# Performance work log

Measured on AMD Instinct MI355X. Metric: run time of the kernel, lower is better.

## Reference

```python
import jax, jax.numpy as jnp
import numpy as np

NUM_HEADS = 32
ROPE_BASE = 10000.0


def _rotate_half(x):
    h = x.shape[-1] // 2
    return jnp.concatenate([-x[..., h:], x[..., :h]], axis=-1)


def setup_inputs() -> dict:
    key = jax.random.key(0)
    ks = jax.random.split(key, 6)
    B, S, H = 2, 2048, 4096
    hidden_states = jax.random.normal(ks[0], (B, S, H), dtype=jnp.float32)
    # additive causal mask: 0 on/below diagonal, large negative above
    causal = jnp.tril(jnp.ones((S, S), dtype=bool))
    attention_mask = jnp.where(causal, 0.0, -1e9).astype(jnp.float32)
    attention_mask = jnp.broadcast_to(attention_mask[None, None], (B, 1, S, S))
    position_ids = jnp.broadcast_to(jnp.arange(S, dtype=jnp.int64 if jax.config.jax_enable_x64 else jnp.int32)[None, :], (B, S))
    scale = 1.0 / np.sqrt(H)
    Wq = jax.random.normal(ks[1], (H, H), dtype=jnp.float32) * scale
    Wk = jax.random.normal(ks[2], (H, H), dtype=jnp.float32) * scale
    Wv = jax.random.normal(ks[3], (H, H), dtype=jnp.float32) * scale
    Wo = jax.random.normal(ks[4], (H, H), dtype=jnp.float32) * scale
    return {"hidden_states": hidden_states, "attention_mask": attention_mask,
            "position_ids": position_ids, "Wq": Wq, "Wk": Wk, "Wv": Wv, "Wo": Wo}


def reference(hidden_states, attention_mask, position_ids, Wq, Wk, Wv, Wo):
    B, S, H = hidden_states.shape
    nh = NUM_HEADS
    hd = H // nh
    # QKV projections (torch Linear: y = x @ W.T), split heads -> [B, nh, S, hd]
    def proj(W):
        y = jnp.einsum('bsh,oh->bso', hidden_states, W)
        return y.reshape(B, S, nh, hd).transpose(0, 2, 1, 3)
    q, k, v = proj(Wq), proj(Wk), proj(Wv)
    # rotary embeddings gathered at position_ids
    inv_freq = 1.0 / (ROPE_BASE ** (jnp.arange(0, hd, 2, dtype=jnp.float32) / hd))
    freqs = position_ids.astype(jnp.float32)[:, :, None] * inv_freq[None, None, :]  # [B,S,hd/2]
    emb = jnp.concatenate([freqs, freqs], axis=-1)  # [B,S,hd]
    cos = jnp.cos(emb)[:, None, :, :]  # [B,1,S,hd]
    sin = jnp.sin(emb)[:, None, :, :]
    q = q * cos + _rotate_half(q) * sin
    k = k * cos + _rotate_half(k) * sin
    # scaled dot-product attention
    scores = jnp.einsum('bhqd,bhkd->bhqk', q, k) / jnp.sqrt(jnp.float32(hd))
    scores = scores + attention_mask
    scores = jnp.maximum(scores, jnp.finfo(scores.dtype).min)
    attn = jax.nn.softmax(scores, axis=-1)
    out = jnp.einsum('bhqk,bhkd->bhqd', attn, v)  # [B,nh,S,hd]
    out = out.transpose(0, 2, 1, 3).reshape(B, S, H)
    return jnp.einsum('bsh,oh->bso', out, Wo)
```

## Files before the change

kernel.cpp:

```cpp
#include <hip/hip_runtime.h>
#include <cstdint>
#include <cmath>

typedef __bf16 bf16;
typedef __bf16 bf16x8 __attribute__((ext_vector_type(8)));
typedef __bf16 bf16x4 __attribute__((ext_vector_type(4)));
typedef float f32x4 __attribute__((ext_vector_type(4)));

#define B_ 2
#define S_ 2048
#define H_ 4096
#define NH 32
#define HD 128

#define VMCNT(n) asm volatile("s_waitcnt vmcnt(" #n ")" ::: "memory")
#define BAR() __builtin_amdgcn_s_barrier()

__device__ __forceinline__ void gl_lds16(const void* g, void* l) {
  __builtin_amdgcn_global_load_lds(
      (const __attribute__((address_space(1))) unsigned int*)g,
      (__attribute__((address_space(3))) unsigned int*)l, 16, 0, 0);
}

__global__ __launch_bounds__(256) void cast_kernel(const float* __restrict__ in,
                                                   bf16* __restrict__ out, int n4) {
  int i = blockIdx.x * 256 + threadIdx.x;
  if (i < n4) {
    float4 v = ((const float4*)in)[i];
    bf16x4 o = {(bf16)v.x, (bf16)v.y, (bf16)v.z, (bf16)v.w};
    ((bf16x4*)out)[i] = o;
  }
}

template <int TM, int TN>
__device__ __forceinline__ void mfma_quad(f32x4 (&acc)[8][4], bf16x8 (&af)[4][2],
                                          bf16x8 (&bfr)[2][2]) {
  __builtin_amdgcn_s_setprio(1);
#pragma unroll
  for (int i = 0; i < 4; ++i)
#pragma unroll
    for (int j = 0; j < 2; ++j)
#pragma unroll
      for (int kf = 0; kf < 2; ++kf)
        acc[TM * 4 + i][TN * 2 + j] = __builtin_amdgcn_mfma_f32_16x16x32_bf16(
            af[i][kf], bfr[j][kf], acc[TM * 4 + i][TN * 2 + j], 0, 0, 0);
  __builtin_amdgcn_s_setprio(0);
}

template <int EPI>
__global__ __launch_bounds__(512, 2) void gemm256(const bf16* __restrict__ A,
                                                  const bf16* __restrict__ Bw,
                                                  void* __restrict__ Cout) {
  constexpr int K = 4096, N = 4096, KT = K / 64;
  __shared__ __attribute__((aligned(16))) char lds[131072];
  char* Al = lds;
  char* Bl = lds + 65536;
  int tid = threadIdx.x;
  int l = tid & 63, lr = l & 15, lg = l >> 4;
  int w = tid >> 6, wm = w >> 2, wn = w & 3;
  int bid = (int)blockIdx.x;
  int swb = (bid & 7) * 32 + (bid >> 3);
  int r0 = (swb >> 4) * 256, c0 = (swb & 15) * 256;
  const bf16* Ab = A + (size_t)r0 * K;
  const bf16* Bb = Bw + (size_t)c0 * K;

  int lr0 = tid >> 3;
  int cel = (((tid & 7) ^ ((tid >> 3) & 7)) << 3);

  auto stageA = [&](int buf, int mh, int k0) {
    char* dst = Al + buf * 32768 + mh * 16384 + tid * 16;
    int ra = mh * 64 + lr0;
    gl_lds16(Ab + (size_t)ra * K + k0 + cel, dst);
    gl_lds16(Ab + (size_t)(ra + 128) * K + k0 + cel, dst + 8192);
  };
  auto stageB = [&](int buf, int nh, int k0) {
    char* dst = Bl + buf * 32768 + nh * 16384 + tid * 16;
    int n0 = (lr0 >> 5) * 64 + nh * 32 + (lr0 & 31);
    gl_lds16(Bb + (size_t)n0 * K + k0 + cel, dst);
    gl_lds16(Bb + (size_t)(n0 + 128) * K + k0 + cel, dst + 8192);
  };

  bf16x8 af[4][2], bfr[2][2];
  int rsw = (lr & 7) << 4;
  auto ldA = [&](int buf, int mh) {
    char* base = Al + buf * 32768 + mh * 16384 + wm * 8192;
#pragma unroll
    for (int mfl = 0; mfl < 4; ++mfl)
#pragma unroll
      for (int kf = 0; kf < 2; ++kf)
        __builtin_memcpy(&af[mfl][kf],
                         base + (mfl * 16 + lr) * 128 + ((kf * 64 + lg * 16) ^ rsw), 16);
  };
  auto ldB = [&](int buf, int nh) {
    char* base = Bl + buf * 32768 + nh * 16384 + wn * 4096;
#pragma unroll
    for (int nfl = 0; nfl < 2; ++nfl)
#pragma unroll
      for (int kf = 0; kf < 2; ++kf)
        __builtin_memcpy(&bfr[nfl][kf],
                         base + (nfl * 16 + lr) * 128 + ((kf * 64 + lg * 16) ^ rsw), 16);
  };

  f32x4 acc[8][4] = {};

  stageA(0, 0, 0);
  stageB(0, 0, 0);
  stageB(0, 1, 0);
  stageA(0, 1, 0);

  for (int kt = 0; kt < KT - 1; ++kt) {
    int buf = kt & 1, nb = buf ^ 1;
    int k0n = (kt + 1) * 64;
    VMCNT(4); BAR();
    ldA(buf, 0); ldB(buf, 0);
    stageA(nb, 0, k0n);
    mfma_quad<0, 0>(acc, af, bfr);
    BAR();
    VMCNT(4); BAR();
    ldB(buf, 1);
    stageB(nb, 0, k0n);
    mfma_quad<0, 1>(acc, af, bfr);
    BAR();
    VMCNT(4); BAR();
    ldA(buf, 1);
    stageB(nb, 1, k0n);
    mfma_quad<1, 1>(acc, af, bfr);
    BAR();
    BAR();
    ldB(buf, 0);
    stageA(nb, 1, k0n);
    mfma_quad<1, 0>(acc, af, bfr);
    BAR();
  }
  {
    int buf = (KT - 1) & 1;
    VMCNT(4); BAR();
    ldA(buf, 0); ldB(buf, 0);
    mfma_quad<0, 0>(acc, af, bfr);
    BAR();
    VMCNT(2); BAR();
    ldB(buf, 1);
    mfma_quad<0, 1>(acc, af, bfr);
    BAR();
    VMCNT(0); BAR();
    ldA(buf, 1);
    mfma_quad<1, 1>(acc, af, bfr);
    BAR();
    BAR();
    ldB(buf, 0);
    mfma_quad<1, 0>(acc, af, bfr);
  }

#pragma unroll
  for (int mf = 0; mf < 8; ++mf)
#pragma unroll
    for (int nf = 0; nf < 4; ++nf) {
      int orow = r0 + wm * 128 + mf * 16 + lg * 4;
      int ocol = c0 + wn * 64 + nf * 16 + lr;
      if (EPI == 0) {
        bf16* C = (bf16*)Cout;
#pragma unroll
        for (int jr = 0; jr < 4; ++jr)
          C[(size_t)(orow + jr) * N + ocol] = (bf16)acc[mf][nf][jr];
      } else {
        float* C = (float*)Cout;
#pragma unroll
        for (int jr = 0; jr < 4; ++jr)
          C[(size_t)(orow + jr) * N + ocol] = acc[mf][nf][jr];
      }
    }
}

__global__ __launch_bounds__(256) void rope_kernel(bf16* __restrict__ Qx,
                                                   bf16* __restrict__ Kx,
                                                   const int* __restrict__ pos,
                                                   float qscale) {
  int r = blockIdx.x;
  bf16* X = blockIdx.y ? Kx : Qx;
  float scale = blockIdx.y ? 1.0f : qscale;
  float pf = (float)pos[r];
  int i = threadIdx.x & 63;
  int h0 = threadIdx.x >> 6;
  float ang = pf * exp2f(-0.20762050593046868f * (float)i);
  float sn = sinf(ang), cs = cosf(ang);
  bf16* row = X + (size_t)r * H_;
#pragma unroll
  for (int h = h0; h < NH; h += 4) {
    bf16* p = row + h * HD + i;
    float a = (float)p[0], b = (float)p[64];
    p[0] = (bf16)((a * cs - b * sn) * scale);
    p[64] = (bf16)((b * cs + a * sn) * scale);
  }
}

__global__ __launch_bounds__(256) void transpose_v(const bf16* __restrict__ V,
                                                   bf16* __restrict__ Vt) {
  __shared__ __attribute__((aligned(16))) bf16 tile[64][130];
  int bh = blockIdx.y;
  int b = bh >> 5, h = bh & 31;
  int s0 = blockIdx.x * 64;
  int t = threadIdx.x;
  const bf16* src = V + (size_t)(b * S_ + s0) * H_ + h * HD;
  int rr = t >> 4, cc = (t & 15) * 8;
#pragma unroll
  for (int k = 0; k < 4; ++k) {
    bf16x8 v;
    __builtin_memcpy(&v, src + (size_t)(rr + k * 16) * H_ + cc, 16);
#pragma unroll
    for (int u = 0; u < 8; ++u) tile[rr + k * 16][cc + u] = v[u];
  }
  __syncthreads();
  bf16* dst = Vt + (size_t)bh * HD * S_;
  int sl = t & 63, d0 = t >> 6;
  for (int j = 0; j < 32; ++j) {
    int d = d0 + j * 4;
    dst[(size_t)d * S_ + s0 + sl] = tile[sl][d];
  }
}

__global__ __launch_bounds__(512, 4) void attn_kernel(const bf16* __restrict__ Q,
                                                      const bf16* __restrict__ Km,
                                                      const bf16* __restrict__ Vt,
                                                      bf16* __restrict__ Out) {
  __shared__ __attribute__((aligned(16))) bf16 Ks[2][64 * 128];
  __shared__ __attribute__((aligned(16))) bf16 Vs[2][128 * 64];
  __shared__ __attribute__((aligned(16))) bf16 P_lds[8][16 * 64];
  int tid = threadIdx.x;
  int w = tid >> 6, l = tid & 63;
  int lr = l & 15, lg = l >> 4;
  int bh = blockIdx.y, b = bh >> 5, h = bh & 31;
  int qt = 15 - (int)blockIdx.x;
  int q0w = qt * 128 + w * 16;
  const bf16* Qb = Q + (size_t)b * S_ * H_ + h * HD;
  const char* Kg = (const char*)(Km + (size_t)b * S_ * H_ + h * HD);
  const char* Vg = (const char*)(Vt + (size_t)bh * HD * S_);
  bf16* Ob = Out + (size_t)b * S_ * H_ + h * HD;

  bf16x8 qf[4];
#pragma unroll
  for (int dk = 0; dk < 4; ++dk)
    __builtin_memcpy(&qf[dk], Qb + (size_t)(q0w + lr) * H_ + dk * 32 + lg * 8, 16);

  f32x4 o[8] = {};
  float m = -INFINITY, ls = 0.f;
  int nkv_blk = 2 * qt + 2;
  int nkv_w = 2 * qt + (w >> 2) + 1;

  auto stageK = [&](int buf, int kv0) {
#pragma unroll
    for (int p = 0; p < 2; ++p) {
      int row = p * 32 + (tid >> 4);
      int src = ((tid & 15) * 16) ^ ((row & 7) << 4);
      gl_lds16(Kg + (size_t)(kv0 + row) * (H_ * 2) + src,
               (char*)&Ks[buf][0] + p * 8192 + w * 1024);
    }
  };
  auto stageV = [&](int buf, int kv0) {
#pragma unroll
    for (int p = 0; p < 2; ++p) {
      int row = p * 64 + (tid >> 3);
      int src = ((tid & 7) * 16) ^ ((row & 7) << 4);
      gl_lds16(Vg + (size_t)row * (S_ * 2) + (size_t)kv0 * 2 + src,
               (char*)&Vs[buf][0] + p * 8192 + w * 1024);
    }
  };

  stageK(0, 0);
  stageV(0, 0);
  __syncthreads();

  int cur = 0;
  char* Pl = (char*)&P_lds[w][0];
  for (int t = 0; t < nkv_blk; ++t) {
    int kv0 = t * 64;
    if (t + 1 < nkv_blk) {
      stageK(cur ^ 1, kv0 + 64);
      stageV(cur ^ 1, kv0 + 64);
    }
    if (t < nkv_w) {
      const char* Kl = (const char*)&Ks[cur][0];
      const char* Vl = (const char*)&Vs[cur][0];
      f32x4 s4[4] = {};
      __builtin_amdgcn_s_setprio(1);
#pragma unroll
      for (int dk = 0; dk < 4; ++dk)
#pragma unroll
        for (int st = 0; st < 4; ++st) {
          int row = st * 16 + lr;
          int cb = (dk * 64 + lg * 16) ^ ((row & 7) << 4);
          bf16x8 kf;
          __builtin_memcpy(&kf, Kl + row * 256 + cb, 16);
          s4[st] = __builtin_amdgcn_mfma_f32_16x16x32_bf16(kf, qf[dk], s4[st], 0, 0, 0);
        }
      __builtin_amdgcn_s_setprio(0);
      if (t == nkv_w - 1) {
        int qg = q0w + lr;
#pragma unroll
        for (int st = 0; st < 4; ++st)
#pragma unroll
          for (int j = 0; j < 4; ++j)
            if (kv0 + st * 16 + lg * 4 + j > qg) s4[st][j] = -INFINITY;
      }
      float mx = -INFINITY;
#pragma unroll
      for (int st = 0; st < 4; ++st)
#pragma unroll
        for (int j = 0; j < 4; ++j) mx = fmaxf(mx, s4[st][j]);
      mx = fmaxf(mx, __shfl_xor(mx, 16));
      mx = fmaxf(mx, __shfl_xor(mx, 32));
      float sc = 1.0f;
      if (!__all((int)(mx <= m + 8.0f))) {
        float mn = fmaxf(m, mx);
        sc = exp2f(m - mn);
        m = mn;
        float scq0 = __shfl(sc, lg * 4 + 0);
        float scq1 = __shfl(sc, lg * 4 + 1);
        float scq2 = __shfl(sc, lg * 4 + 2);
        float scq3 = __shfl(sc, lg * 4 + 3);
#pragma unroll
        for (int dt = 0; dt < 8; ++dt) {
          o[dt][0] *= scq0; o[dt][1] *= scq1; o[dt][2] *= scq2; o[dt][3] *= scq3;
        }
      }
      float pv[4][4], rs = 0.f;
#pragma unroll
      for (int st = 0; st < 4; ++st)
#pragma unroll
        for (int j = 0; j < 4; ++j) {
          pv[st][j] = exp2f(s4[st][j] - m);
          rs += pv[st][j];
        }
      rs += __shfl_xor(rs, 16);
      rs += __shfl_xor(rs, 32);
      ls = ls * sc + rs;
#pragma unroll
      for (int st = 0; st < 4; ++st) {
        bf16x4 pk = {(bf16)pv[st][0], (bf16)pv[st][1], (bf16)pv[st][2], (bf16)pv[st][3]};
        *(bf16x4*)(Pl + lr * 128 + ((st * 32 + lg * 8) ^ ((lr & 7) << 4))) = pk;
      }
      bf16x8 pa[2];
#pragma unroll
      for (int ks = 0; ks < 2; ++ks)
        __builtin_memcpy(&pa[ks], Pl + lr * 128 + ((ks * 64 + lg * 16) ^ ((lr & 7) << 4)), 16);
      __builtin_amdgcn_s_setprio(1);
#pragma unroll
      for (int dt = 0; dt < 8; ++dt)
#pragma unroll
        for (int ks = 0; ks < 2; ++ks) {
          int row = dt * 16 + lr;
          int cb = (ks * 64 + lg * 16) ^ ((row & 7) << 4);
          bf16x8 vf;
          __builtin_memcpy(&vf, Vl + row * 128 + cb, 16);
          o[dt] = __builtin_amdgcn_mfma_f32_16x16x32_bf16(pa[ks], vf, o[dt], 0, 0, 0);
        }
      __builtin_amdgcn_s_setprio(0);
    }
    __syncthreads();
    cur ^= 1;
  }
  float lsq[4];
#pragma unroll
  for (int j = 0; j < 4; ++j) lsq[j] = __shfl(ls, lg * 4 + j);
#pragma unroll
  for (int j = 0; j < 4; ++j) {
    float inv = 1.0f / lsq[j];
#pragma unroll
    for (int dt = 0; dt < 8; ++dt)
      Ob[(size_t)(q0w + lg * 4 + j) * H_ + dt * 16 + lr] = (bf16)(o[dt][j] * inv);
  }
}

extern "C" void kernel_launch(void* const* d_in, const int* in_sizes, int n_in,
                              void* d_out, int out_size, void* d_ws, size_t ws_size,
                              hipStream_t stream) {
  const float* X = (const float*)d_in[0];
  const int* pos = (const int*)d_in[2];
  const float* Wq = (const float*)d_in[3];
  const float* Wk = (const float*)d_in[4];
  const float* Wv = (const float*)d_in[5];
  const float* Wo = (const float*)d_in[6];
  float* out = (float*)d_out;
  char* ws = (char*)d_ws;
  const size_t MB32 = 32ull << 20;
  bf16* Xb = (bf16*)ws;
  bf16* Wb = (bf16*)(ws + MB32);
  bf16* Qb = (bf16*)(ws + 2 * MB32);
  bf16* Kb = (bf16*)(ws + 3 * MB32);
  bf16* Vb = (bf16*)(ws + 4 * MB32);
  bf16* Vt = (bf16*)(ws + 5 * MB32);

  const int n4 = (4096 * 4096) / 4;
  dim3 cgrid(n4 / 256), cblk(256);
  dim3 ggrid(256), gblk(512);

  cast_kernel<<<cgrid, cblk, 0, stream>>>(X, Xb, n4);
  cast_kernel<<<cgrid, cblk, 0, stream>>>(Wq, Wb, n4);
  gemm256<0><<<ggrid, gblk, 0, stream>>>(Xb, Wb, Qb);
  cast_kernel<<<cgrid, cblk, 0, stream>>>(Wk, Wb, n4);
  gemm256<0><<<ggrid, gblk, 0, stream>>>(Xb, Wb, Kb);
  cast_kernel<<<cgrid, cblk, 0, stream>>>(Wv, Wb, n4);
  gemm256<0><<<ggrid, gblk, 0, stream>>>(Xb, Wb, Vb);

  const float qscale = 1.4426950408889634f / 11.313708498984760f;
  rope_kernel<<<dim3(4096, 2), 256, 0, stream>>>(Qb, Kb, pos, qscale);
  transpose_v<<<dim3(32, 64), 256, 0, stream>>>(Vb, Vt);

  attn_kernel<<<dim3(16, 64), 512, 0, stream>>>(Qb, Kb, Vt, Xb);

  cast_kernel<<<cgrid, cblk, 0, stream>>>(Wo, Wb, n4);
  gemm256<1><<<ggrid, gblk, 0, stream>>>(Xb, Wb, out);
}
```

Measured before the change: 888.5 us.

## Keep both B fragment halves in registers and cut GEMM barriers per k-step

The GEMM main loop now holds two B fragment sets (bf0, bf1), so the last quadrant reuses bf0 and no longer reloads B from LDS. The barrier and vmcnt schedule is restructured to drop several barriers per k-tile, and LDS reads are issued ahead of the previous MFMA block's completion. The goal is less LDS read traffic and fewer synchronization stalls. In exchange it adds register pressure, and the weaker barrier and waitcnt ordering risks LDS races with the async global-to-LDS staging.

```diff
diff --git a/kernel.cpp b/kernel.cpp
--- a/kernel.cpp
+++ b/kernel.cpp
@@ -33,8 +33,8 @@
 }
 
 template <int TM, int TN>
-__device__ __forceinline__ void mfma_quad(f32x4 (&acc)[8][4], bf16x8 (&af)[4][2],
-                                          bf16x8 (&bfr)[2][2]) {
+__device__ __forceinline__ void mfma_q(f32x4 (&acc)[8][4], bf16x8 (&a)[4][2],
+                                       bf16x8 (&b)[2][2]) {
   __builtin_amdgcn_s_setprio(1);
 #pragma unroll
   for (int i = 0; i < 4; ++i)
@@ -43,7 +43,7 @@
 #pragma unroll
       for (int kf = 0; kf < 2; ++kf)
         acc[TM * 4 + i][TN * 2 + j] = __builtin_amdgcn_mfma_f32_16x16x32_bf16(
-            af[i][kf], bfr[j][kf], acc[TM * 4 + i][TN * 2 + j], 0, 0, 0);
+            a[i][kf], b[j][kf], acc[TM * 4 + i][TN * 2 + j], 0, 0, 0);
   __builtin_amdgcn_s_setprio(0);
 }
 
@@ -80,27 +80,27 @@
     gl_lds16(Bb + (size_t)(n0 + 128) * K + k0 + cel, dst + 8192);
   };
 
-  bf16x8 af[4][2], bfr[2][2];
   int rsw = (lr & 7) << 4;
-  auto ldA = [&](int buf, int mh) {
+  auto ldA = [&](bf16x8 (&dst)[4][2], int buf, int mh) {
     char* base = Al + buf * 32768 + mh * 16384 + wm * 8192;
 #pragma unroll
     for (int mfl = 0; mfl < 4; ++mfl)
 #pragma unroll
       for (int kf = 0; kf < 2; ++kf)
-        __builtin_memcpy(&af[mfl][kf],
+        __builtin_memcpy(&dst[mfl][kf],
                          base + (mfl * 16 + lr) * 128 + ((kf * 64 + lg * 16) ^ rsw), 16);
   };
-  auto ldB = [&](int buf, int nh) {
+  auto ldB = [&](bf16x8 (&dst)[2][2], int buf, int nh) {
     char* base = Bl + buf * 32768 + nh * 16384 + wn * 4096;
 #pragma unroll
     for (int nfl = 0; nfl < 2; ++nfl)
 #pragma unroll
       for (int kf = 0; kf < 2; ++kf)
-        __builtin_memcpy(&bfr[nfl][kf],
+        __builtin_memcpy(&dst[nfl][kf],
                          base + (nfl * 16 + lr) * 128 + ((kf * 64 + lg * 16) ^ rsw), 16);
   };
 
+  bf16x8 af[4][2], bf0[2][2], bf1[2][2];
   f32x4 acc[8][4] = {};
 
   stageA(0, 0, 0);
@@ -111,44 +111,38 @@
   for (int kt = 0; kt < KT - 1; ++kt) {
     int buf = kt & 1, nb = buf ^ 1;
     int k0n = (kt + 1) * 64;
-    VMCNT(4); BAR();
-    ldA(buf, 0); ldB(buf, 0);
+    VMCNT(2); BAR();
+    ldA(af, buf, 0);
+    ldB(bf0, buf, 0);
     stageA(nb, 0, k0n);
-    mfma_quad<0, 0>(acc, af, bfr);
+    mfma_q<0, 0>(acc, af, bf0);
+    ldB(bf1, buf, 1);
+    VMCNT(2);
     BAR();
-    VMCNT(4); BAR();
-    ldB(buf, 1);
     stageB(nb, 0, k0n);
-    mfma_quad<0, 1>(acc, af, bfr);
+    mfma_q<0, 1>(acc, af, bf1);
+    ldA(af, buf, 1);
     BAR();
-    VMCNT(4); BAR();
-    ldA(buf, 1);
     stageB(nb, 1, k0n);
-    mfma_quad<1, 1>(acc, af, bfr);
+    mfma_q<1, 1>(acc, af, bf1);
     BAR();
-    BAR();
-    ldB(buf, 0);
     stageA(nb, 1, k0n);
-    mfma_quad<1, 0>(acc, af, bfr);
-    BAR();
+    mfma_q<1, 0>(acc, af, bf0);
   }
   {
     int buf = (KT - 1) & 1;
-    VMCNT(4); BAR();
-    ldA(buf, 0); ldB(buf, 0);
-    mfma_quad<0, 0>(acc, af, bfr);
+    VMCNT(2); BAR();
+    ldA(af, buf, 0);
+    ldB(bf0, buf, 0);
+    mfma_q<0, 0>(acc, af, bf0);
+    ldB(bf1, buf, 1);
+    VMCNT(0);
     BAR();
-    VMCNT(2); BAR();
-    ldB(buf, 1);
-    mfma_quad<0, 1>(acc, af, bfr);
+    mfma_q<0, 1>(acc, af, bf1);
+    ldA(af, buf, 1);
     BAR();
-    VMCNT(0); BAR();
-    ldA(buf, 1);
-    mfma_quad<1, 1>(acc, af, bfr);
-    BAR();
-    BAR();
-    ldB(buf, 0);
-    mfma_quad<1, 0>(acc, af, bfr);
+    mfma_q<1, 1>(acc, af, bf1);
+    mfma_q<1, 0>(acc, af, bf0);
   }
 
 #pragma unroll
```

After: 880.1 us. About the same (-0.9%).

## Restructure GEMM main loop into k-half phases with deeper prefetch

Applied to the files above, without the earlier changes.

Reorganizes the 256x256 bf16 GEMM mainloop so each LDS buffer holds two 32-wide k-slices, and each phase loads 8 A fragments and 2 B fragments and issues 16 MFMAs per half of N. Global-to-LDS staging now runs two k-tiles ahead instead of one, which is meant to hide load latency better. The XOR swizzle on LDS is removed in favour of a plain 64-byte row layout, which risks LDS bank conflicts on the fragment reads. It also adds more barriers per iteration.

```diff
diff --git a/kernel.cpp b/kernel.cpp
--- a/kernel.cpp
+++ b/kernel.cpp
@@ -32,18 +32,16 @@
   }
 }
 
-template <int TM, int TN>
-__device__ __forceinline__ void mfma_quad(f32x4 (&acc)[8][4], bf16x8 (&af)[4][2],
-                                          bf16x8 (&bfr)[2][2]) {
+template <int TNH>
+__device__ __forceinline__ void mfma_ph(f32x4 (&acc)[8][4], bf16x8 (&a)[8],
+                                        bf16x8 (&b)[2]) {
   __builtin_amdgcn_s_setprio(1);
 #pragma unroll
-  for (int i = 0; i < 4; ++i)
-#pragma unroll
-    for (int j = 0; j < 2; ++j)
-#pragma unroll
-      for (int kf = 0; kf < 2; ++kf)
-        acc[TM * 4 + i][TN * 2 + j] = __builtin_amdgcn_mfma_f32_16x16x32_bf16(
-            af[i][kf], bfr[j][kf], acc[TM * 4 + i][TN * 2 + j], 0, 0, 0);
+  for (int mf = 0; mf < 8; ++mf)
+#pragma unroll
+    for (int nf = 0; nf < 2; ++nf)
+      acc[mf][TNH * 2 + nf] = __builtin_amdgcn_mfma_f32_16x16x32_bf16(
+          a[mf], b[nf], acc[mf][TNH * 2 + nf], 0, 0, 0);
   __builtin_amdgcn_s_setprio(0);
 }
 
@@ -64,91 +62,100 @@
   const bf16* Ab = A + (size_t)r0 * K;
   const bf16* Bb = Bw + (size_t)c0 * K;
 
-  int lr0 = tid >> 3;
-  int cel = (((tid & 7) ^ ((tid >> 3) & 7)) << 3);
-
-  auto stageA = [&](int buf, int mh, int k0) {
-    char* dst = Al + buf * 32768 + mh * 16384 + tid * 16;
-    int ra = mh * 64 + lr0;
-    gl_lds16(Ab + (size_t)ra * K + k0 + cel, dst);
-    gl_lds16(Ab + (size_t)(ra + 128) * K + k0 + cel, dst + 8192);
-  };
-  auto stageB = [&](int buf, int nh, int k0) {
-    char* dst = Bl + buf * 32768 + nh * 16384 + tid * 16;
-    int n0 = (lr0 >> 5) * 64 + nh * 32 + (lr0 & 31);
-    gl_lds16(Bb + (size_t)n0 * K + k0 + cel, dst);
-    gl_lds16(Bb + (size_t)(n0 + 128) * K + k0 + cel, dst + 8192);
-  };
-
-  bf16x8 af[4][2], bfr[2][2];
-  int rsw = (lr & 7) << 4;
-  auto ldA = [&](int buf, int mh) {
-    char* base = Al + buf * 32768 + mh * 16384 + wm * 8192;
-#pragma unroll
-    for (int mfl = 0; mfl < 4; ++mfl)
-#pragma unroll
-      for (int kf = 0; kf < 2; ++kf)
-        __builtin_memcpy(&af[mfl][kf],
-                         base + (mfl * 16 + lr) * 128 + ((kf * 64 + lg * 16) ^ rsw), 16);
-  };
-  auto ldB = [&](int buf, int nh) {
-    char* base = Bl + buf * 32768 + nh * 16384 + wn * 4096;
-#pragma unroll
-    for (int nfl = 0; nfl < 2; ++nfl)
-#pragma unroll
-      for (int kf = 0; kf < 2; ++kf)
-        __builtin_memcpy(&bfr[nfl][kf],
-                         base + (nfl * 16 + lr) * 128 + ((kf * 64 + lg * 16) ^ rsw), 16);
+  int srow = tid >> 2;
+  int scol = (tid & 3) * 8;
+
+  auto stageA = [&](int u, int kk) {
+    char* dst = Al + (u & 1) * 32768 + kk * 16384 + tid * 16;
+    int k0 = u * 64 + kk * 32 + scol;
+    gl_lds16(Ab + (size_t)srow * K + k0, dst);
+    gl_lds16(Ab + (size_t)(srow + 128) * K + k0, dst + 8192);
+  };
+  auto stageB = [&](int u, int kk) {
+    char* dst = Bl + (u & 1) * 32768 + kk * 16384 + tid * 16;
+    int k0 = u * 64 + kk * 32 + scol;
+    gl_lds16(Bb + (size_t)srow * K + k0, dst);
+    gl_lds16(Bb + (size_t)(srow + 128) * K + k0, dst + 8192);
+  };
+
+  bf16x8 a[8], b[2];
+  auto ldA8 = [&](int u, int kk) {
+    char* base = Al + (u & 1) * 32768 + kk * 16384 + (wm * 128 + lr) * 64 + lg * 16;
+#pragma unroll
+    for (int mf = 0; mf < 8; ++mf) __builtin_memcpy(&a[mf], base + mf * 1024, 16);
+  };
+  auto ldB2 = [&](int u, int kk, int nh) {
+    char* base = Bl + (u & 1) * 32768 + kk * 16384 + (wn * 64 + nh * 32 + lr) * 64 + lg * 16;
+#pragma unroll
+    for (int nf = 0; nf < 2; ++nf) __builtin_memcpy(&b[nf], base + nf * 1024, 16);
   };
 
   f32x4 acc[8][4] = {};
 
-  stageA(0, 0, 0);
-  stageB(0, 0, 0);
-  stageB(0, 1, 0);
-  stageA(0, 1, 0);
-
-  for (int kt = 0; kt < KT - 1; ++kt) {
-    int buf = kt & 1, nb = buf ^ 1;
-    int k0n = (kt + 1) * 64;
+  stageA(0, 0); stageB(0, 0); stageA(0, 1); stageB(0, 1);
+  stageA(1, 0); stageB(1, 0); stageA(1, 1);
+  VMCNT(10);
+  BAR();
+
+  for (int u = 0; u < KT - 2; ++u) {
+    ldA8(u, 0); ldB2(u, 0, 0);
+    stageB(u + 1, 1);
+    BAR();
+    mfma_ph<0>(acc, a, b);
+    BAR();
+    ldB2(u, 0, 1);
+    stageA(u + 2, 0);
+    BAR();
+    mfma_ph<1>(acc, a, b);
+    VMCNT(10); BAR();
+    ldA8(u, 1); ldB2(u, 1, 0);
+    stageB(u + 2, 0);
+    BAR();
+    mfma_ph<0>(acc, a, b);
+    BAR();
+    ldB2(u, 1, 1);
+    stageA(u + 2, 1);
+    BAR();
+    mfma_ph<1>(acc, a, b);
+    VMCNT(10); BAR();
+  }
+  {
+    int u = KT - 2;
+    ldA8(u, 0); ldB2(u, 0, 0);
+    stageB(u + 1, 1);
+    BAR();
+    mfma_ph<0>(acc, a, b);
+    BAR();
+    ldB2(u, 0, 1);
+    BAR();
+    mfma_ph<1>(acc, a, b);
+    VMCNT(8); BAR();
+    ldA8(u, 1); ldB2(u, 1, 0);
+    BAR();
+    mfma_ph<0>(acc, a, b);
+    BAR();
+    ldB2(u, 1, 1);
+    BAR();
+    mfma_ph<1>(acc, a, b);
     VMCNT(4); BAR();
-    ldA(buf, 0); ldB(buf, 0);
-    stageA(nb, 0, k0n);
-    mfma_quad<0, 0>(acc, af, bfr);
-    BAR();
-    VMCNT(4); BAR();
-    ldB(buf, 1);
-    stageB(nb, 0, k0n);
-    mfma_quad<0, 1>(acc, af, bfr);
-    BAR();
-    VMCNT(4); BAR();
-    ldA(buf, 1);
-    stageB(nb, 1, k0n);
-    mfma_quad<1, 1>(acc, af, bfr);
-    BAR();
-    BAR();
-    ldB(buf, 0);
-    stageA(nb, 1, k0n);
-    mfma_quad<1, 0>(acc, af, bfr);
-    BAR();
   }
   {
-    int buf = (KT - 1) & 1;
-    VMCNT(4); BAR();
-    ldA(buf, 0); ldB(buf, 0);
-    mfma_quad<0, 0>(acc, af, bfr);
-    BAR();
-    VMCNT(2); BAR();
-    ldB(buf, 1);
-    mfma_quad<0, 1>(acc, af, bfr);
-    BAR();
+    int u = KT - 1;
+    ldA8(u, 0); ldB2(u, 0, 0);
+    BAR();
+    mfma_ph<0>(acc, a, b);
+    BAR();
+    ldB2(u, 0, 1);
+    BAR();
+    mfma_ph<1>(acc, a, b);
     VMCNT(0); BAR();
-    ldA(buf, 1);
-    mfma_quad<1, 1>(acc, af, bfr);
-    BAR();
-    BAR();
-    ldB(buf, 0);
-    mfma_quad<1, 0>(acc, af, bfr);
+    ldA8(u, 1); ldB2(u, 1, 0);
+    BAR();
+    mfma_ph<0>(acc, a, b);
+    BAR();
+    ldB2(u, 1, 1);
+    BAR();
+    mfma_ph<1>(acc, a, b);
   }
 
 #pragma unroll
```

Result: slower. 967.3 us (+8.9%).
